# Kernel optimization log

Hardware: AMD Instinct MI355X
Metric: run time of the kernel (lower is better)

## Reference

```python
import jax, jax.numpy as jnp
import numpy as np

DIM = 1024

def _circ_conv(x, key):
    # circular convolution along last dim via FFT
    D = x.shape[-1]
    return jnp.fft.irfft(jnp.fft.rfft(x, axis=-1) * jnp.fft.rfft(key), n=D, axis=-1)

def _circ_corr(x, key):
    # circular correlation: conjugate the key spectrum
    D = x.shape[-1]
    return jnp.fft.irfft(jnp.fft.rfft(x, axis=-1) * jnp.conj(jnp.fft.rfft(key)), n=D, axis=-1)

def setup_inputs() -> dict:
    key = jax.random.key(0)
    k0, k1, k2 = jax.random.split(key, 3)
    B, T, D = 4, 2048, DIM
    x = jax.random.normal(k0, (B, T, D), dtype=jnp.float32)
    bind_key = jax.random.normal(k1, (D,), dtype=jnp.float32) * 0.02
    unbind_key = jax.random.normal(k2, (D,), dtype=jnp.float32) * 0.02
    gate = jnp.ones((1,), dtype=jnp.float32)
    decay = jnp.asarray(0.9, dtype=jnp.float32)
    return {"x": x, "bind_key": bind_key, "unbind_key": unbind_key, "gate": gate, "decay": decay}

def reference(x, bind_key, unbind_key, gate, decay):
    B, T, D = x.shape
    bound = _circ_conv(x, bind_key)                      # (B, T, D)
    d = jax.nn.sigmoid(decay)
    pos = jnp.arange(T, dtype=x.dtype)
    diff = pos[:, None] - pos[None, :]                   # (T, T)
    causal = diff >= 0
    # clamp exponent to avoid inf*0 on masked (t < s) entries; math identical to tril mask
    decay_matrix = jnp.where(causal, d ** jnp.maximum(diff, 0.0), 0.0)
    hologram = jnp.einsum('ts,bsd->btd', decay_matrix, bound)
    retrieved = _circ_corr(hologram, unbind_key)
    return x + gate * retrieved
```

## Files before the change

### kernel.cpp

```cpp
#include <hip/hip_runtime.h>
#include <hip/hip_bf16.h>

constexpr int Dd = 1024;
constexpr int Tt = 2048;
constexpr int Bb = 4;
constexpr int Rr = Bb * Tt;
constexpr int NCH = 64;
constexpr int CL  = 32;
constexpr int SCB = Bb * NCH;
constexpr int CBL = 64;
constexpr int WBL = 512;

typedef __attribute__((ext_vector_type(4))) float f32x4;
typedef __attribute__((ext_vector_type(8))) short bf16x8;

__device__ __forceinline__ float sigmoidf_(float v) {
    return 1.0f / (1.0f + expf(-v));
}

__device__ __forceinline__ short bf16bits(float f) {
    union { __hip_bfloat16 b; short s; } u;
    u.b = __float2bfloat16(f);
    return u.s;
}

__device__ __forceinline__ void async16(const void* g, void* l) {
    __builtin_amdgcn_global_load_lds(
        (const __attribute__((address_space(1))) unsigned int*)g,
        (__attribute__((address_space(3))) unsigned int*)l,
        16, 0, 0);
}

__global__ void k_endc(const float* __restrict__ x,
                       const float* __restrict__ bind,
                       const float* __restrict__ unbind,
                       const float* __restrict__ decay,
                       float* __restrict__ endv,
                       float* __restrict__ c) {
    __shared__ float sb[Dd];
    __shared__ float su[Dd];
    __shared__ float sp[256];

    const int tid = threadIdx.x;
    if (blockIdx.x < SCB) {
        const int chunk = blockIdx.x & (NCH - 1);
        const int b = blockIdx.x >> 6;
        const float dd = sigmoidf_(decay[0]);
        const size_t base = ((size_t)b * Tt + (size_t)chunk * CL) * Dd + tid * 4;
        f32x4 e = (f32x4){0.f, 0.f, 0.f, 0.f};
        #pragma unroll 8
        for (int t = 0; t < CL; ++t) {
            f32x4 v = *(const f32x4*)&x[base + (size_t)t * Dd];
            e = dd * e + v;
        }
        *(f32x4*)&endv[((size_t)b * NCH + chunk) * Dd + tid * 4] = e;
    } else {
        for (int j = tid; j < Dd; j += 256) { sb[j] = bind[j]; su[j] = unbind[j]; }
        __syncthreads();
        const int n_loc = tid >> 4;
        const int seg = tid & 15;
        const int n = (int)(blockIdx.x - SCB) * 16 + n_loc;
        float acc = 0.f;
        #pragma unroll 8
        for (int i = 0; i < 64; ++i) {
            const int m = i * 16 + seg;
            acc = fmaf(su[m], sb[(m + n) & (Dd - 1)], acc);
        }
        sp[tid] = acc;
        __syncthreads();
        if (tid < 16) {
            float s = 0.f;
            #pragma unroll
            for (int j = 0; j < 16; ++j) s += sp[tid * 16 + j];
            c[(int)(blockIdx.x - SCB) * 16 + tid] = s;
        }
    }
}

__global__ void k_scanw(const float* __restrict__ x,
                        const float* __restrict__ c,
                        const float* __restrict__ decay,
                        const float* __restrict__ endv,
                        __hip_bfloat16* __restrict__ xs,
                        __hip_bfloat16* __restrict__ wt) {
    const int tid = threadIdx.x;
    if (blockIdx.x < SCB) {
        const int chunk = blockIdx.x & (NCH - 1);
        const int b = blockIdx.x >> 6;
        const float dd = sigmoidf_(decay[0]);
        const float dL = powf(dd, (float)CL);
        f32x4 h = (f32x4){0.f, 0.f, 0.f, 0.f};
        const float* ep = endv + ((size_t)b * NCH) * Dd + tid * 4;
        for (int cc = 0; cc < chunk; ++cc)
            h = dL * h + *(const f32x4*)&ep[(size_t)cc * Dd];
        const size_t base = ((size_t)b * Tt + (size_t)chunk * CL) * Dd + tid * 4;
        #pragma unroll 8
        for (int t = 0; t < CL; ++t) {
            f32x4 v = *(const f32x4*)&x[base + (size_t)t * Dd];
            h = dd * h + v;
            short4 o;
            o.x = bf16bits(h[0]); o.y = bf16bits(h[1]);
            o.z = bf16bits(h[2]); o.w = bf16bits(h[3]);
            *(short4*)&xs[base + (size_t)t * Dd] = o;
        }
    } else {
        const int idx8 = (int)(blockIdx.x - SCB) * 256 + tid;
        const int n = idx8 >> 7;
        const int k0 = (idx8 & 127) * 8;
        bf16x8 v;
        #pragma unroll
        for (int j = 0; j < 8; ++j)
            v[j] = bf16bits(c[(n - (k0 + j)) & (Dd - 1)]);
        *(bf16x8*)&wt[(size_t)n * Dd + k0] = v;
    }
}

__global__ __launch_bounds__(256) void k_gemm(
    const __hip_bfloat16* __restrict__ A,
    const __hip_bfloat16* __restrict__ Wt,
    const float* __restrict__ x,
    const float* __restrict__ gate,
    float* __restrict__ out)
{
    __shared__ __align__(16) __hip_bfloat16 sA[128 * 32];
    __shared__ __align__(16) __hip_bfloat16 sB[128 * 32];

    const int tid = threadIdx.x;
    const int wave = tid >> 6;
    const int lane = tid & 63;
    const int tile_m = blockIdx.x * 128;
    const int tile_n = blockIdx.y * 128;
    const int wm = (wave & 1) * 64;
    const int wn = (wave >> 1) * 64;

    f32x4 acc[4][4];
    #pragma unroll
    for (int i = 0; i < 4; ++i)
        #pragma unroll
        for (int j = 0; j < 4; ++j)
            acc[i][j] = (f32x4){0.f, 0.f, 0.f, 0.f};

    const int srow = lane >> 2;
    const int skk  = (lane & 3) * 8;
    const int fr = lane & 15;
    const int fk = (lane >> 4) * 8;

    for (int k0 = 0; k0 < Dd; k0 += 32) {
        __syncthreads();
        #pragma unroll
        for (int j = 0; j < 2; ++j) {
            const int row = wave * 32 + j * 16;
            async16(A  + (size_t)(tile_m + row + srow) * Dd + k0 + skk, &sA[row * 32]);
            async16(Wt + (size_t)(tile_n + row + srow) * Dd + k0 + skk, &sB[row * 32]);
        }
        __syncthreads();

        bf16x8 af[4], bfr[4];
        #pragma unroll
        for (int mt = 0; mt < 4; ++mt)
            af[mt] = *(const bf16x8*)&sA[(wm + mt * 16 + fr) * 32 + fk];
        #pragma unroll
        for (int nt = 0; nt < 4; ++nt)
            bfr[nt] = *(const bf16x8*)&sB[(wn + nt * 16 + fr) * 32 + fk];

        #pragma unroll
        for (int mt = 0; mt < 4; ++mt)
            #pragma unroll
            for (int nt = 0; nt < 4; ++nt)
                acc[mt][nt] = __builtin_amdgcn_mfma_f32_16x16x32_bf16(
                    af[mt], bfr[nt], acc[mt][nt], 0, 0, 0);
    }

    const float g = gate[0];
    #pragma unroll
    for (int mt = 0; mt < 4; ++mt) {
        const int row0 = tile_m + wm + mt * 16 + (lane >> 4) * 4;
        #pragma unroll
        for (int nt = 0; nt < 4; ++nt) {
            const int col = tile_n + wn + nt * 16 + (lane & 15);
            #pragma unroll
            for (int gg = 0; gg < 4; ++gg) {
                const size_t off = (size_t)(row0 + gg) * Dd + col;
                out[off] = fmaf(g, acc[mt][nt][gg], x[off]);
            }
        }
    }
}

extern "C" void kernel_launch(void* const* d_in, const int* in_sizes, int n_in,
                              void* d_out, int out_size, void* d_ws, size_t ws_size,
                              hipStream_t stream) {
    const float* x      = (const float*)d_in[0];
    const float* bind   = (const float*)d_in[1];
    const float* unbind = (const float*)d_in[2];
    const float* gate   = (const float*)d_in[3];
    const float* decay  = (const float*)d_in[4];
    float* out = (float*)d_out;

    char* ws = (char*)d_ws;
    __hip_bfloat16* wt = (__hip_bfloat16*)ws;
    __hip_bfloat16* xs = (__hip_bfloat16*)(ws + (size_t)Dd * Dd * 2);
    float* endv = (float*)(ws + (size_t)Dd * Dd * 2 + (size_t)Rr * Dd * 2);
    float* c    = endv + (size_t)Bb * NCH * Dd;

    k_endc <<<dim3(SCB + CBL), dim3(256), 0, stream>>>(x, bind, unbind, decay, endv, c);
    k_scanw<<<dim3(SCB + WBL), dim3(256), 0, stream>>>(x, c, decay, endv, xs, wt);
    k_gemm <<<dim3(64, 8),     dim3(256), 0, stream>>>(xs, wt, x, gate, out);
}
```

Baseline: 134.3 us.

## Fuse scan, weight build and GEMM into one cooperative persistent kernel

Merges the three launches into a single cooperative kernel with grid-wide syncs between the chunk-end scan, the prefix/weight-build phase and the bf16 MFMA GEMM. Chunk length is halved to 16, giving 512 blocks that match the 128-tile GEMM grid. This removes inter-kernel launch gaps and tail idling, at the cost of grid barrier overhead, a longer serial carry loop over chunk ends, and a bigger endv workspace. A fallback to the three-kernel path is kept if the cooperative launch fails.

After: 277.6 us. +106.7%, slower.

```diff
diff --git a/kernel.cpp b/kernel.cpp
--- a/kernel.cpp
+++ b/kernel.cpp
@@ -1,15 +1,17 @@
 #include <hip/hip_runtime.h>
 #include <hip/hip_bf16.h>
+#include <hip/hip_cooperative_groups.h>
+
+namespace cg = cooperative_groups;
 
 constexpr int Dd = 1024;
 constexpr int Tt = 2048;
 constexpr int Bb = 4;
 constexpr int Rr = Bb * Tt;
-constexpr int NCH = 64;
-constexpr int CL  = 32;
-constexpr int SCB = Bb * NCH;
+constexpr int NCH = 128;
+constexpr int CL  = 16;
+constexpr int GRID = 512;
 constexpr int CBL = 64;
-constexpr int WBL = 512;
 
 typedef __attribute__((ext_vector_type(4))) float f32x4;
 typedef __attribute__((ext_vector_type(8))) short bf16x8;
@@ -29,6 +31,186 @@
         (const __attribute__((address_space(1))) unsigned int*)g,
         (__attribute__((address_space(3))) unsigned int*)l,
         16, 0, 0);
+}
+
+
+__device__ __forceinline__ void p1_scan_end(const float* __restrict__ x,
+                                            float dd, int b, int ch, int tid,
+                                            float* __restrict__ endv) {
+    const size_t base = ((size_t)b * Tt + (size_t)ch * CL) * Dd + tid * 4;
+    f32x4 e = (f32x4){0.f, 0.f, 0.f, 0.f};
+    #pragma unroll
+    for (int t = 0; t < CL; ++t) {
+        f32x4 v = *(const f32x4*)&x[base + (size_t)t * Dd];
+        e = dd * e + v;
+    }
+    *(f32x4*)&endv[((size_t)b * NCH + ch) * Dd + tid * 4] = e;
+}
+
+__device__ __forceinline__ void p1_cblock(const float* __restrict__ bind,
+                                          const float* __restrict__ unbind,
+                                          int cb, int tid,
+                                          float* sb, float* su, float* sp,
+                                          float* __restrict__ c) {
+    for (int j = tid; j < Dd; j += 256) { sb[j] = bind[j]; su[j] = unbind[j]; }
+    __syncthreads();
+    const int n_loc = tid >> 4;
+    const int seg = tid & 15;
+    const int n = cb * 16 + n_loc;
+    float acc = 0.f;
+    #pragma unroll 8
+    for (int i = 0; i < 64; ++i) {
+        const int m = i * 16 + seg;
+        acc = fmaf(su[m], sb[(m + n) & (Dd - 1)], acc);
+    }
+    sp[tid] = acc;
+    __syncthreads();
+    if (tid < 16) {
+        float s = 0.f;
+        #pragma unroll
+        for (int j = 0; j < 16; ++j) s += sp[tid * 16 + j];
+        c[cb * 16 + tid] = s;
+    }
+}
+
+__device__ __forceinline__ void p2_scan_write(const float* __restrict__ x,
+                                              float dd, int b, int ch, int tid,
+                                              const float* __restrict__ endv,
+                                              __hip_bfloat16* __restrict__ xs) {
+    const float dL = powf(dd, (float)CL);
+    f32x4 h = (f32x4){0.f, 0.f, 0.f, 0.f};
+    const float* ep = endv + ((size_t)b * NCH) * Dd + tid * 4;
+    #pragma unroll 8
+    for (int cc = 0; cc < ch; ++cc)
+        h = dL * h + *(const f32x4*)&ep[(size_t)cc * Dd];
+    const size_t base = ((size_t)b * Tt + (size_t)ch * CL) * Dd + tid * 4;
+    #pragma unroll
+    for (int t = 0; t < CL; ++t) {
+        f32x4 v = *(const f32x4*)&x[base + (size_t)t * Dd];
+        h = dd * h + v;
+        short4 o;
+        o.x = bf16bits(h[0]); o.y = bf16bits(h[1]);
+        o.z = bf16bits(h[2]); o.w = bf16bits(h[3]);
+        *(short4*)&xs[base + (size_t)t * Dd] = o;
+    }
+}
+
+__device__ __forceinline__ void p2_wbuild(const float* __restrict__ c,
+                                          int wb, int tid,
+                                          __hip_bfloat16* __restrict__ wt) {
+    const int idx8 = wb * 256 + tid;
+    const int n = idx8 >> 7;
+    const int k0 = (idx8 & 127) * 8;
+    bf16x8 v;
+    #pragma unroll
+    for (int j = 0; j < 8; ++j)
+        v[j] = bf16bits(c[(n - (k0 + j)) & (Dd - 1)]);
+    *(bf16x8*)&wt[(size_t)n * Dd + k0] = v;
+}
+
+__device__ __forceinline__ void p3_gemm_tile(const __hip_bfloat16* __restrict__ A,
+                                             const __hip_bfloat16* __restrict__ Wt,
+                                             const float* __restrict__ x,
+                                             float g, int tile_m, int tile_n,
+                                             int tid,
+                                             __hip_bfloat16* sA, __hip_bfloat16* sB,
+                                             float* __restrict__ out) {
+    const int wave = tid >> 6;
+    const int lane = tid & 63;
+    const int wm = (wave & 1) * 64;
+    const int wn = (wave >> 1) * 64;
+
+    f32x4 acc[4][4];
+    #pragma unroll
+    for (int i = 0; i < 4; ++i)
+        #pragma unroll
+        for (int j = 0; j < 4; ++j)
+            acc[i][j] = (f32x4){0.f, 0.f, 0.f, 0.f};
+
+    const int srow = lane >> 2;
+    const int skk  = (lane & 3) * 8;
+    const int fr = lane & 15;
+    const int fk = (lane >> 4) * 8;
+
+    for (int k0 = 0; k0 < Dd; k0 += 32) {
+        __syncthreads();
+        #pragma unroll
+        for (int j = 0; j < 2; ++j) {
+            const int row = wave * 32 + j * 16;
+            async16(A  + (size_t)(tile_m + row + srow) * Dd + k0 + skk, &sA[row * 32]);
+            async16(Wt + (size_t)(tile_n + row + srow) * Dd + k0 + skk, &sB[row * 32]);
+        }
+        __syncthreads();
+
+        bf16x8 af[4], bfr[4];
+        #pragma unroll
+        for (int mt = 0; mt < 4; ++mt)
+            af[mt] = *(const bf16x8*)&sA[(wm + mt * 16 + fr) * 32 + fk];
+        #pragma unroll
+        for (int nt = 0; nt < 4; ++nt)
+            bfr[nt] = *(const bf16x8*)&sB[(wn + nt * 16 + fr) * 32 + fk];
+
+        #pragma unroll
+        for (int mt = 0; mt < 4; ++mt)
+            #pragma unroll
+            for (int nt = 0; nt < 4; ++nt)
+                acc[mt][nt] = __builtin_amdgcn_mfma_f32_16x16x32_bf16(
+                    af[mt], bfr[nt], acc[mt][nt], 0, 0, 0);
+    }
+
+    #pragma unroll
+    for (int mt = 0; mt < 4; ++mt) {
+        const int row0 = tile_m + wm + mt * 16 + (lane >> 4) * 4;
+        #pragma unroll
+        for (int nt = 0; nt < 4; ++nt) {
+            const int col = tile_n + wn + nt * 16 + (lane & 15);
+            #pragma unroll
+            for (int gg = 0; gg < 4; ++gg) {
+                const size_t off = (size_t)(row0 + gg) * Dd + col;
+                out[off] = fmaf(g, acc[mt][nt][gg], x[off]);
+            }
+        }
+    }
+}
+
+__global__ __launch_bounds__(256, 2) void k_mega(
+    const float* __restrict__ x,
+    const float* __restrict__ bind,
+    const float* __restrict__ unbind,
+    const float* __restrict__ gate,
+    const float* __restrict__ decay,
+    float* __restrict__ out,
+    __hip_bfloat16* __restrict__ wt,
+    __hip_bfloat16* __restrict__ xs,
+    float* __restrict__ endv,
+    float* __restrict__ c)
+{
+    __shared__ __align__(16) char smem[128 * 32 * 2 * 2];
+    __hip_bfloat16* sA = (__hip_bfloat16*)smem;
+    __hip_bfloat16* sB = (__hip_bfloat16*)(smem + 128 * 32 * 2);
+    float* sb = (float*)smem;
+    float* su = (float*)(smem + 4096);
+    float* sp = (float*)(smem + 8192);
+
+    const int tid = threadIdx.x;
+    const int blk = blockIdx.x;
+    const float dd = sigmoidf_(decay[0]);
+    const int ch = blk & (NCH - 1);
+    const int b  = blk >> 7;
+
+    p1_scan_end(x, dd, b, ch, tid, endv);
+    if (blk >= GRID - CBL)
+        p1_cblock(bind, unbind, blk - (GRID - CBL), tid, sb, su, sp, c);
+
+    cg::this_grid().sync();
+
+    p2_scan_write(x, dd, b, ch, tid, endv, xs);
+    p2_wbuild(c, blk, tid, wt);
+
+    cg::this_grid().sync();
+
+    p3_gemm_tile(xs, wt, x, gate[0], (blk & 63) * 128, (blk >> 6) * 128,
+                 tid, sA, sB, out);
 }
 
 __global__ void k_endc(const float* __restrict__ x,
@@ -40,40 +222,12 @@
     __shared__ float sb[Dd];
     __shared__ float su[Dd];
     __shared__ float sp[256];
-
     const int tid = threadIdx.x;
-    if (blockIdx.x < SCB) {
-        const int chunk = blockIdx.x & (NCH - 1);
-        const int b = blockIdx.x >> 6;
-        const float dd = sigmoidf_(decay[0]);
-        const size_t base = ((size_t)b * Tt + (size_t)chunk * CL) * Dd + tid * 4;
-        f32x4 e = (f32x4){0.f, 0.f, 0.f, 0.f};
-        #pragma unroll 8
-        for (int t = 0; t < CL; ++t) {
-            f32x4 v = *(const f32x4*)&x[base + (size_t)t * Dd];
-            e = dd * e + v;
-        }
-        *(f32x4*)&endv[((size_t)b * NCH + chunk) * Dd + tid * 4] = e;
+    const float dd = sigmoidf_(decay[0]);
+    if (blockIdx.x < GRID) {
+        p1_scan_end(x, dd, blockIdx.x >> 7, blockIdx.x & (NCH - 1), tid, endv);
     } else {
-        for (int j = tid; j < Dd; j += 256) { sb[j] = bind[j]; su[j] = unbind[j]; }
-        __syncthreads();
-        const int n_loc = tid >> 4;
-        const int seg = tid & 15;
-        const int n = (int)(blockIdx.x - SCB) * 16 + n_loc;
-        float acc = 0.f;
-        #pragma unroll 8
-        for (int i = 0; i < 64; ++i) {
-            const int m = i * 16 + seg;
-            acc = fmaf(su[m], sb[(m + n) & (Dd - 1)], acc);
-        }
-        sp[tid] = acc;
-        __syncthreads();
-        if (tid < 16) {
-            float s = 0.f;
-            #pragma unroll
-            for (int j = 0; j < 16; ++j) s += sp[tid * 16 + j];
-            c[(int)(blockIdx.x - SCB) * 16 + tid] = s;
-        }
+        p1_cblock(bind, unbind, (int)blockIdx.x - GRID, tid, sb, su, sp, c);
     }
 }
 
@@ -84,34 +238,11 @@
                         __hip_bfloat16* __restrict__ xs,
                         __hip_bfloat16* __restrict__ wt) {
     const int tid = threadIdx.x;
-    if (blockIdx.x < SCB) {
-        const int chunk = blockIdx.x & (NCH - 1);
-        const int b = blockIdx.x >> 6;
+    if (blockIdx.x < GRID) {
         const float dd = sigmoidf_(decay[0]);
-        const float dL = powf(dd, (float)CL);
-        f32x4 h = (f32x4){0.f, 0.f, 0.f, 0.f};
-        const float* ep = endv + ((size_t)b * NCH) * Dd + tid * 4;
-        for (int cc = 0; cc < chunk; ++cc)
-            h = dL * h + *(const f32x4*)&ep[(size_t)cc * Dd];
-        const size_t base = ((size_t)b * Tt + (size_t)chunk * CL) * Dd + tid * 4;
-        #pragma unroll 8
-        for (int t = 0; t < CL; ++t) {
-            f32x4 v = *(const f32x4*)&x[base + (size_t)t * Dd];
-            h = dd * h + v;
-            short4 o;
-            o.x = bf16bits(h[0]); o.y = bf16bits(h[1]);
-            o.z = bf16bits(h[2]); o.w = bf16bits(h[3]);
-            *(short4*)&xs[base + (size_t)t * Dd] = o;
-        }
+        p2_scan_write(x, dd, blockIdx.x >> 7, blockIdx.x & (NCH - 1), tid, endv, xs);
     } else {
-        const int idx8 = (int)(blockIdx.x - SCB) * 256 + tid;
-        const int n = idx8 >> 7;
-        const int k0 = (idx8 & 127) * 8;
-        bf16x8 v;
-        #pragma unroll
-        for (int j = 0; j < 8; ++j)
-            v[j] = bf16bits(c[(n - (k0 + j)) & (Dd - 1)]);
-        *(bf16x8*)&wt[(size_t)n * Dd + k0] = v;
+        p2_wbuild(c, (int)blockIdx.x - GRID, tid, wt);
     }
 }
 
@@ -120,71 +251,11 @@
     const __hip_bfloat16* __restrict__ Wt,
     const float* __restrict__ x,
     const float* __restrict__ gate,
-    float* __restrict__ out)
-{
+    float* __restrict__ out) {
     __shared__ __align__(16) __hip_bfloat16 sA[128 * 32];
     __shared__ __align__(16) __hip_bfloat16 sB[128 * 32];
-
-    const int tid = threadIdx.x;
-    const int wave = tid >> 6;
-    const int lane = tid & 63;
-    const int tile_m = blockIdx.x * 128;
-    const int tile_n = blockIdx.y * 128;
-    const int wm = (wave & 1) * 64;
-    const int wn = (wave >> 1) * 64;
-
-    f32x4 acc[4][4];
-    #pragma unroll
-    for (int i = 0; i < 4; ++i)
-        #pragma unroll
-        for (int j = 0; j < 4; ++j)
-            acc[i][j] = (f32x4){0.f, 0.f, 0.f, 0.f};
-
-    const int srow = lane >> 2;
-    const int skk  = (lane & 3) * 8;
-    const int fr = lane & 15;
-    const int fk = (lane >> 4) * 8;
-
-    for (int k0 = 0; k0 < Dd; k0 += 32) {
-        __syncthreads();
-        #pragma unroll
-        for (int j = 0; j < 2; ++j) {
-            const int row = wave * 32 + j * 16;
-            async16(A  + (size_t)(tile_m + row + srow) * Dd + k0 + skk, &sA[row * 32]);
-            async16(Wt + (size_t)(tile_n + row + srow) * Dd + k0 + skk, &sB[row * 32]);
-        }
-        __syncthreads();
-
-        bf16x8 af[4], bfr[4];
-        #pragma unroll
-        for (int mt = 0; mt < 4; ++mt)
-            af[mt] = *(const bf16x8*)&sA[(wm + mt * 16 + fr) * 32 + fk];
-        #pragma unroll
-        for (int nt = 0; nt < 4; ++nt)
-            bfr[nt] = *(const bf16x8*)&sB[(wn + nt * 16 + fr) * 32 + fk];
-
-        #pragma unroll
-        for (int mt = 0; mt < 4; ++mt)
-            #pragma unroll
-            for (int nt = 0; nt < 4; ++nt)
-                acc[mt][nt] = __builtin_amdgcn_mfma_f32_16x16x32_bf16(
-                    af[mt], bfr[nt], acc[mt][nt], 0, 0, 0);
-    }
-
-    const float g = gate[0];
-    #pragma unroll
-    for (int mt = 0; mt < 4; ++mt) {
-        const int row0 = tile_m + wm + mt * 16 + (lane >> 4) * 4;
-        #pragma unroll
-        for (int nt = 0; nt < 4; ++nt) {
-            const int col = tile_n + wn + nt * 16 + (lane & 15);
-            #pragma unroll
-            for (int gg = 0; gg < 4; ++gg) {
-                const size_t off = (size_t)(row0 + gg) * Dd + col;
-                out[off] = fmaf(g, acc[mt][nt][gg], x[off]);
-            }
-        }
-    }
+    p3_gemm_tile(A, Wt, x, gate[0], blockIdx.x * 128, blockIdx.y * 128,
+                 threadIdx.x, sA, sB, out);
 }
 
 extern "C" void kernel_launch(void* const* d_in, const int* in_sizes, int n_in,
@@ -203,7 +274,15 @@
     float* endv = (float*)(ws + (size_t)Dd * Dd * 2 + (size_t)Rr * Dd * 2);
     float* c    = endv + (size_t)Bb * NCH * Dd;
 
-    k_endc <<<dim3(SCB + CBL), dim3(256), 0, stream>>>(x, bind, unbind, decay, endv, c);
-    k_scanw<<<dim3(SCB + WBL), dim3(256), 0, stream>>>(x, c, decay, endv, xs, wt);
-    k_gemm <<<dim3(64, 8),     dim3(256), 0, stream>>>(xs, wt, x, gate, out);
-}
+    void* args[] = {
+        (void*)&x, (void*)&bind, (void*)&unbind, (void*)&gate, (void*)&decay,
+        (void*)&out, (void*)&wt, (void*)&xs, (void*)&endv, (void*)&c
+    };
+    hipError_t err = hipLaunchCooperativeKernel((const void*)k_mega, dim3(GRID),
+                                                dim3(256), args, 0, stream);
+    if (err != hipSuccess) {
+        k_endc <<<dim3(GRID + CBL),  dim3(256), 0, stream>>>(x, bind, unbind, decay, endv, c);
+        k_scanw<<<dim3(GRID + GRID), dim3(256), 0, stream>>>(x, c, decay, endv, xs, wt);
+        k_gemm <<<dim3(64, 8),       dim3(256), 0, stream>>>(xs, wt, x, gate, out);
+    }
+}
```
